# Performance work log

Measured on AMD Instinct MI355X. Metric: run time of the kernel, lower is better.

The kernel has to match this reference:

```python
import jax, jax.numpy as jnp
import numpy as np
from functools import partial

IM_H, IM_W = 1024, 1024
PRE_NMS = 1000
POST_NMS = 1000
FPN_POST_NMS = 1000
NMS_THRESH = 0.7
MIN_SIZE = 0.0
XFORM_CLIP = float(np.log(1000.0 / 16.0))  # BoxCoder bbox_xform_clip
K_MIN, K_MAX, K0, S0 = 2, 5, 4, 224.0      # ROI->FPN level mapper
NEG_INF = -1.0e30
N_IMG = 8


def _make_anchors(H, W, stride, n_img):
    """Grid anchors in H,W,A order (matches permute(0,2,3,1) flattening)."""
    ratios = np.array([0.5, 1.0, 2.0])
    size = stride * 8.0
    ws = size * np.sqrt(1.0 / ratios)
    hs = size * np.sqrt(ratios)
    sx = (np.arange(W) + 0.5) * stride
    sy = (np.arange(H) + 0.5) * stride
    cx, cy = np.meshgrid(sx, sy)  # [H,W]
    x1 = cx[..., None] - ws / 2.0
    y1 = cy[..., None] - hs / 2.0
    x2 = cx[..., None] + ws / 2.0
    y2 = cy[..., None] + hs / 2.0
    anc = np.stack([x1, y1, x2, y2], -1).reshape(-1, 4).astype(np.float32)
    return jnp.asarray(np.broadcast_to(anc, (n_img,) + anc.shape).copy())


def setup_inputs() -> dict:
    key = jax.random.key(0)
    ks = jax.random.split(key, 6)
    inp = {
        "obj_p2": jax.random.normal(ks[0], (N_IMG, 3, 256, 256), jnp.float32),
        "obj_p3": jax.random.normal(ks[1], (N_IMG, 3, 128, 128), jnp.float32),
        "obj_p4": jax.random.normal(ks[2], (N_IMG, 3, 64, 64), jnp.float32),
        "breg_p2": jax.random.normal(ks[3], (N_IMG, 12, 256, 256), jnp.float32) * 0.25,
        "breg_p3": jax.random.normal(ks[4], (N_IMG, 12, 128, 128), jnp.float32) * 0.25,
        "breg_p4": jax.random.normal(ks[5], (N_IMG, 12, 64, 64), jnp.float32) * 0.25,
        "anchors_p2": _make_anchors(256, 256, 4, N_IMG),
        "anchors_p3": _make_anchors(128, 128, 8, N_IMG),
        "anchors_p4": _make_anchors(64, 64, 16, N_IMG),
    }
    return inp


def _decode(deltas, anchors):
    # BoxCoder(weights=(1,1,1,1)) decode with the detectron +1 convention
    w = anchors[..., 2] - anchors[..., 0] + 1.0
    h = anchors[..., 3] - anchors[..., 1] + 1.0
    cx = anchors[..., 0] + 0.5 * w
    cy = anchors[..., 1] + 0.5 * h
    dx, dy = deltas[..., 0], deltas[..., 1]
    dw = jnp.minimum(deltas[..., 2], XFORM_CLIP)
    dh = jnp.minimum(deltas[..., 3], XFORM_CLIP)
    pcx = dx * w + cx
    pcy = dy * h + cy
    pw = jnp.exp(dw) * w
    ph = jnp.exp(dh) * h
    return jnp.stack(
        [pcx - 0.5 * pw, pcy - 0.5 * ph, pcx + 0.5 * pw - 1.0, pcy + 0.5 * ph - 1.0], -1
    )


def _nms_keep(boxes, valid, thresh):
    # boxes [K,4] already sorted by score desc; greedy hard NMS -> keep mask
    x1, y1, x2, y2 = boxes[:, 0], boxes[:, 1], boxes[:, 2], boxes[:, 3]
    areas = (x2 - x1 + 1.0) * (y2 - y1 + 1.0)
    xx1 = jnp.maximum(x1[:, None], x1[None, :])
    yy1 = jnp.maximum(y1[:, None], y1[None, :])
    xx2 = jnp.minimum(x2[:, None], x2[None, :])
    yy2 = jnp.minimum(y2[:, None], y2[None, :])
    inter = jnp.clip(xx2 - xx1 + 1.0, 0.0) * jnp.clip(yy2 - yy1 + 1.0, 0.0)
    iou = inter / (areas[:, None] + areas[None, :] - inter)
    K = boxes.shape[0]
    js = jnp.arange(K)

    def body(i, keep):
        sup = keep[i] & (iou[i] > thresh) & (js > i)
        return keep & ~sup

    return jax.lax.fori_loop(0, K, body, valid)


def _per_level(obj, breg, anchors):
    N, A, H, W = obj.shape
    scores = jax.nn.sigmoid(obj.transpose(0, 2, 3, 1).reshape(N, -1))  # [N, HWA]
    deltas = breg.reshape(N, A, 4, H, W).transpose(0, 3, 4, 1, 2).reshape(N, -1, 4)
    k = min(PRE_NMS, scores.shape[1])
    s, idx = jax.lax.top_k(scores, k)  # sorted desc
    d = jnp.take_along_axis(deltas, idx[..., None], axis=1)
    a = jnp.take_along_axis(anchors, idx[..., None], axis=1)
    p = _decode(d, a)
    # clip to image (width-1 / height-1)
    p = jnp.stack(
        [
            jnp.clip(p[..., 0], 0.0, IM_W - 1.0),
            jnp.clip(p[..., 1], 0.0, IM_H - 1.0),
            jnp.clip(p[..., 2], 0.0, IM_W - 1.0),
            jnp.clip(p[..., 3], 0.0, IM_H - 1.0),
        ],
        -1,
    )
    ws = p[..., 2] - p[..., 0] + 1.0
    hs = p[..., 3] - p[..., 1] + 1.0
    xc = p[..., 0] + ws / 2.0
    yc = p[..., 1] + hs / 2.0
    valid = (ws >= MIN_SIZE) & (hs >= MIN_SIZE) & (xc < IM_W) & (yc < IM_H)
    keep = jax.vmap(partial(_nms_keep, thresh=NMS_THRESH))(p, valid)
    ms = jnp.where(keep, s, NEG_INF)
    s2, i2 = jax.lax.top_k(ms, min(POST_NMS, k))
    b2 = jnp.take_along_axis(p, i2[..., None], axis=1)
    return b2, s2


def reference(obj_p2, obj_p3, obj_p4, breg_p2, breg_p3, breg_p4,
              anchors_p2, anchors_p3, anchors_p4):
    levels_in = [
        (obj_p2, breg_p2, anchors_p2),
        (obj_p3, breg_p3, anchors_p3),
        (obj_p4, breg_p4, anchors_p4),
    ]
    bs, ss = zip(*[_per_level(o, b, a) for o, b, a in levels_in])
    boxes = jnp.concatenate(bs, axis=1)   # [N, L*POST_NMS, 4]
    scores = jnp.concatenate(ss, axis=1)  # [N, L*POST_NMS]
    pk = min(FPN_POST_NMS, scores.shape[1])
    fs, fi = jax.lax.top_k(scores, pk)    # per-image inference-mode topk
    fb = jnp.take_along_axis(boxes, fi[..., None], axis=1)
    # ROI -> FPN level mapping
    area = (fb[..., 2] - fb[..., 0] + 1.0) * (fb[..., 3] - fb[..., 1] + 1.0)
    lvl = jnp.floor(K0 + jnp.log2(jnp.sqrt(area) / S0 + 1e-6))
    lvl = jnp.clip(lvl, K_MIN, K_MAX).astype(jnp.int32)
    return fb, fs, lvl
```

## Files before the change

kernel.cpp:

```cpp
#include <hip/hip_runtime.h>

#define NTASK 24
#define KSEL 1000
#define NIMG 8
#define NEG_INF_D (-1e30)
#define SEG 192
#define SORTN 2048


static __device__ __forceinline__ unsigned fkey(float x) {
    unsigned u = __float_as_uint(x);
    return u ^ ((u >> 31) ? 0xFFFFFFFFu : 0x80000000u);
}

static __device__ __forceinline__ float fkey_inv(unsigned key) {
    unsigned u = (key >> 31) ? (key ^ 0x80000000u) : ~key;
    return __uint_as_float(u);
}

static __device__ __forceinline__ unsigned long long dkey(double d) {
    unsigned long long u = (unsigned long long)__double_as_longlong(d);
    if (u >> 63) u = ~u; else u |= 0x8000000000000000ull;
    return u;
}

static __device__ __forceinline__ int level_hw(int lvl) {
    return lvl == 0 ? 65536 : (lvl == 1 ? 16384 : 4096);
}


__global__ __launch_bounds__(256) void k_zero(uint4* __restrict__ p, int n16) {
    const int t = blockIdx.x * 256 + threadIdx.x;
    if (t < n16) p[t] = make_uint4(0u, 0u, 0u, 0u);
}


__global__ __launch_bounds__(256) void k_hist(const float* __restrict__ o2,
                                              const float* __restrict__ o3,
                                              const float* __restrict__ o4,
                                              unsigned* __restrict__ hist) {
    const int task = blockIdx.x, img = task / 3, lvl = task % 3;
    const float* obj = lvl == 0 ? o2 : (lvl == 1 ? o3 : o4);
    const int HW = level_hw(lvl);
    const int total = 3 * HW;
    const float* base = obj + (size_t)img * total;
    const int tid = threadIdx.x;

    __shared__ unsigned h[4096];
    for (int t = tid; t < 4096; t += 256) h[t] = 0u;
    __syncthreads();

    const int per4 = (total / 32) >> 2;
    const int beg4 = blockIdx.y * per4;
    const float4* base4 = (const float4*)base;
    for (int t = beg4 + tid; t < beg4 + per4; t += 256) {
        float4 v = base4[t];
        atomicAdd(&h[fkey(v.x) >> 20], 1u);
        atomicAdd(&h[fkey(v.y) >> 20], 1u);
        atomicAdd(&h[fkey(v.z) >> 20], 1u);
        atomicAdd(&h[fkey(v.w) >> 20], 1u);
    }
    __syncthreads();

    unsigned* H = hist + task * 4096;
    for (int t = tid; t < 4096; t += 256)
        if (h[t]) atomicAdd(&H[t], h[t]);
}


__global__ __launch_bounds__(256) void k_thresh(const unsigned* __restrict__ hist,
                                                int* __restrict__ thrBin) {
    const int task = blockIdx.x, tid = threadIdx.x;
    __shared__ unsigned h[4096];
    __shared__ unsigned part[256];
    const unsigned* H = hist + task * 4096;
    for (int t = tid; t < 4096; t += 256) h[t] = H[t];
    __syncthreads();
    unsigned s = 0;
    for (int q = 0; q < 16; ++q) s += h[tid * 16 + q];
    part[tid] = s;
    __syncthreads();
    if (tid == 0) {
        unsigned cum = 0;
        int c = 255;
        for (; c >= 0; --c) {
            if (cum + part[c] >= (unsigned)KSEL) break;
            cum += part[c];
        }
        if (c < 0) c = 0;
        int bin = 0;
        for (int b = c * 16 + 15; b >= c * 16; --b) {
            if (cum + h[b] >= (unsigned)KSEL) { bin = b; break; }
            cum += h[b];
        }
        thrBin[task] = bin;
    }
}


__global__ __launch_bounds__(256) void k_compact(const float* __restrict__ o2,
                                                 const float* __restrict__ o3,
                                                 const float* __restrict__ o4,
                                                 const int* __restrict__ thrBin,
                                                 int* __restrict__ cntB,
                                                 unsigned long long* __restrict__ cand) {
    const int task = blockIdx.x, img = task / 3, lvl = task % 3;
    const float* obj = lvl == 0 ? o2 : (lvl == 1 ? o3 : o4);
    const int HW = level_hw(lvl);
    const int total = 3 * HW;
    const float* base = obj + (size_t)img * total;
    const unsigned B = (unsigned)thrBin[task];

    __shared__ unsigned long long buf[256];
    __shared__ unsigned scnt;
    if (threadIdx.x == 0) scnt = 0u;
    __syncthreads();

    const int per4 = (total / 32) >> 2;
    const int beg4 = blockIdx.y * per4;
    const float4* base4 = (const float4*)base;
    for (int t = beg4 + threadIdx.x; t < beg4 + per4; t += 256) {
        float4 v = base4[t];
        const int e0 = t * 4;
#pragma unroll
        for (int q = 0; q < 4; ++q) {
            float x = q == 0 ? v.x : (q == 1 ? v.y : (q == 2 ? v.z : v.w));
            unsigned key = fkey(x);
            if ((key >> 20) >= B) {
                unsigned s = atomicAdd(&scnt, 1u);
                if (s < 256u) {
                    int el = e0 + q;
                    int a = el / HW, pos = el - a * HW;
                    int i = pos * 3 + a;
                    buf[s] = ((unsigned long long)key << 32) | (unsigned)(~(unsigned)i);
                }
            }
        }
    }
    __syncthreads();
    int n = (int)scnt; if (n > SEG) n = SEG;
    const int seg = task * 32 + blockIdx.y;
    if (threadIdx.x == 0) cntB[seg] = n;
    unsigned long long* C = cand + (size_t)seg * SEG;
    for (int t = threadIdx.x; t < n; t += 256) C[t] = buf[t];
}


__global__ __launch_bounds__(1024) void k_sel(const int* __restrict__ cntB,
                                              const unsigned long long* __restrict__ cand,
                                              unsigned long long* __restrict__ sorted64) {
    const int task = blockIdx.x, tid = threadIdx.x;
    const int wid = tid >> 6, lane = tid & 63;
    __shared__ unsigned long long comp[SORTN];
    __shared__ int pref[33];

    if (tid == 0) {
        int p = 0;
        for (int s = 0; s < 32; ++s) { pref[s] = p; p += cntB[task * 32 + s]; }
        pref[32] = p;
    }
    for (int t = tid; t < SORTN; t += 1024) comp[t] = 0ull;
    __syncthreads();

    for (int s = wid; s < 32; s += 16) {
        const int b = pref[s], n = pref[s + 1] - b;
        const unsigned long long* C = cand + (size_t)(task * 32 + s) * SEG;
        for (int k = lane; k < n; k += 64)
            if (b + k < SORTN) comp[b + k] = C[k];
    }
    __syncthreads();

    for (unsigned k = 2; k <= SORTN; k <<= 1) {
        for (unsigned j = k >> 1; j > 0; j >>= 1) {
            for (unsigned i = tid; i < SORTN; i += 1024) {
                unsigned ixj = i ^ j;
                if (ixj > i) {
                    unsigned long long A = comp[i], Bv = comp[ixj];
                    bool desc = ((i & k) == 0);
                    if ((A < Bv) == desc) { comp[i] = Bv; comp[ixj] = A; }
                }
            }
            __syncthreads();
        }
    }

    for (int t = tid; t < KSEL; t += 1024) sorted64[task * KSEL + t] = comp[t];
}


__global__ __launch_bounds__(128) void k_decode(
    const unsigned long long* __restrict__ sorted64,
    const float* __restrict__ g2, const float* __restrict__ g3, const float* __restrict__ g4,
    const float* __restrict__ a2, const float* __restrict__ a3, const float* __restrict__ a4,
    double* __restrict__ boxes, double* __restrict__ score, int* __restrict__ valid) {

    const int task = blockIdx.x, img = task / 3, lvl = task % 3;
    const int r = blockIdx.y * 125 + threadIdx.x;
    if (threadIdx.x >= 125) return;

    const float* brg = lvl == 0 ? g2 : (lvl == 1 ? g3 : g4);
    const float* anc = lvl == 0 ? a2 : (lvl == 1 ? a3 : a4);
    const int HW = level_hw(lvl);
    const int N = HW * 3;
    const double XC = 4.135166556742356;

    unsigned long long e = sorted64[task * KSEL + r];
    unsigned key = (unsigned)(e >> 32);
    int i = (int)(~(unsigned)(e & 0xFFFFFFFFull));
    int a = i % 3, pos = i / 3;

    double x = (double)fkey_inv(key);
    double s = 1.0 / (1.0 + exp(-x));

    const float* bb = brg + (size_t)img * 12 * HW + (size_t)(a * 4) * HW + pos;
    double dx = (double)bb[0];
    double dy = (double)bb[(size_t)HW];
    double dw = (double)bb[(size_t)2 * HW];
    double dh = (double)bb[(size_t)3 * HW];

    const float* an = anc + ((size_t)img * N + (size_t)i) * 4;
    double ax1 = an[0], ay1 = an[1], ax2 = an[2], ay2 = an[3];

    double w = ax2 - ax1 + 1.0, h = ay2 - ay1 + 1.0;
    double cx = ax1 + 0.5 * w, cy = ay1 + 0.5 * h;
    if (dw > XC) dw = XC;
    if (dh > XC) dh = XC;
    double pcx = dx * w + cx, pcy = dy * h + cy;
    double pw = exp(dw) * w, ph = exp(dh) * h;
    double x1 = pcx - 0.5 * pw, y1 = pcy - 0.5 * ph;
    double x2 = pcx + 0.5 * pw - 1.0, y2 = pcy + 0.5 * ph - 1.0;
    x1 = fmin(fmax(x1, 0.0), 1023.0);
    y1 = fmin(fmax(y1, 0.0), 1023.0);
    x2 = fmin(fmax(x2, 0.0), 1023.0);
    y2 = fmin(fmax(y2, 0.0), 1023.0);
    double ws_ = x2 - x1 + 1.0, hs_ = y2 - y1 + 1.0;
    double xc = x1 + ws_ / 2.0, yc = y1 + hs_ / 2.0;
    int v = (ws_ >= 0.0) && (hs_ >= 0.0) && (xc < 1024.0) && (yc < 1024.0);

    double* bo = boxes + (size_t)(task * KSEL + r) * 4;
    bo[0] = x1; bo[1] = y1; bo[2] = x2; bo[3] = y2;
    score[task * KSEL + r] = s;
    valid[task * KSEL + r] = v;
}


__global__ __launch_bounds__(512) void k_mask(const double* __restrict__ boxes,
                                              unsigned long long* __restrict__ maskT) {
    const int task = blockIdx.x;
    const int wid = threadIdx.x >> 6, lane = threadIdx.x & 63;
    const int t = blockIdx.y * 8 + wid;
    if (t >= 136) return;
    int I = 0, rem = t;
    while (rem >= 16 - I) { rem -= 16 - I; ++I; }
    const int J = I + rem;

    const double* B = boxes + (size_t)task * KSEL * 4;
    const int j = J * 64 + lane;
    const int jc = j < KSEL ? j : KSEL - 1;
    double jx1 = B[jc * 4 + 0], jy1 = B[jc * 4 + 1];
    double jx2 = B[jc * 4 + 2], jy2 = B[jc * 4 + 3];
    double aj = (jx2 - jx1 + 1.0) * (jy2 - jy1 + 1.0);

    unsigned long long* MT = maskT + (size_t)task * 16000 + (size_t)J * KSEL;
    int iend = I * 64 + 64; if (iend > KSEL) iend = KSEL;
    for (int i = I * 64; i < iend; ++i) {
        double ix1 = B[i * 4 + 0], iy1 = B[i * 4 + 1];
        double ix2 = B[i * 4 + 2], iy2 = B[i * 4 + 3];
        double ai = (ix2 - ix1 + 1.0) * (iy2 - iy1 + 1.0);
        double xx1 = fmax(ix1, jx1), yy1 = fmax(iy1, jy1);
        double xx2 = fmin(ix2, jx2), yy2 = fmin(iy2, jy2);
        double iw = xx2 - xx1 + 1.0; iw = iw > 0.0 ? iw : 0.0;
        double ih = yy2 - yy1 + 1.0; ih = ih > 0.0 ? ih : 0.0;
        double inter = iw * ih;
        double iou = inter / (ai + aj - inter);
        bool sup = (j > i) && (j < KSEL) && (iou > 0.7);
        unsigned long long m = __ballot(sup);
        if (lane == 0) MT[i] = m;
    }
}


__global__ __launch_bounds__(1024) void k_nms(const unsigned long long* __restrict__ maskT,
                                              const int* __restrict__ valid,
                                              const double* __restrict__ score,
                                              int* __restrict__ order, double* __restrict__ s2) {
    const int task = blockIdx.x;
    const int tid = threadIdx.x;
    const int wid = tid >> 6, lane = tid & 63;

    __shared__ unsigned long long Msh[16000];
    __shared__ unsigned long long kws[16];
    __shared__ int prefK[16], prefN[16], totKsh;

    {
        const ulonglong2* MG = (const ulonglong2*)(maskT + (size_t)task * 16000);
        ulonglong2* ML = (ulonglong2*)Msh;
        for (int t = tid; t < 8000; t += 1024) ML[t] = MG[t];
    }
    if (tid < 16) kws[tid] = 0ull;
    __syncthreads();
    if (tid < KSEL && valid[task * KSEL + tid])
        atomicOr(&kws[tid >> 6], 1ull << (tid & 63));
    __syncthreads();

    for (int p = 0; p < 16; ++p) {
        if (p > 0 && wid >= p) {
            unsigned long long kp = kws[p - 1];
            unsigned long long m = ((kp >> lane) & 1ull) ? Msh[wid * KSEL + (p - 1) * 64 + lane] : 0ull;
            if (m) atomicAnd(&kws[wid], ~m);
        }
        if (wid == p) {
            __threadfence_block();
            const int row = p * 64 + lane;
            unsigned long long m = (row < KSEL) ? Msh[p * KSEL + row] : 0ull;
            unsigned long long k = kws[p];
            unsigned long long processed = 0ull;
            while (true) {
                unsigned long long sup = __ballot((m & k) != 0ull);
                unsigned long long rem = k & sup & ~processed;
                if (!rem) break;
                int b = __ffsll((long long)rem) - 1;
                unsigned lo = (unsigned)__builtin_amdgcn_readlane((int)(unsigned)(m & 0xFFFFFFFFull), b);
                unsigned hi = (unsigned)__builtin_amdgcn_readlane((int)(unsigned)(m >> 32), b);
                unsigned long long vict = ((unsigned long long)hi << 32) | lo;
                k &= ~vict;
                processed = (1ull << b) | ((1ull << b) - 1ull);
            }
            if (lane == 0) kws[p] = k;
        }
        __syncthreads();
    }

    if (tid == 0) {
        int pk = 0, pn = 0;
        for (int l = 0; l < 16; ++l) {
            prefK[l] = pk; prefN[l] = pn;
            int limit = KSEL - 64 * l; if (limit > 64) limit = 64;
            int kb = (int)__popcll(kws[l]);
            pk += kb; pn += limit - kb;
        }
        totKsh = pk;
    }
    __syncthreads();

    if (tid < 16) {
        unsigned long long kw = kws[tid];
        int limit = KSEL - 64 * tid; if (limit > 64) limit = 64;
        int ck = prefK[tid], cn = totKsh + prefN[tid];
        for (int b = 0; b < limit; ++b) {
            int j = tid * 64 + b;
            if ((kw >> b) & 1ull) {
                order[task * KSEL + ck] = j;
                s2[task * KSEL + ck] = score[task * KSEL + j];
                ++ck;
            } else {
                order[task * KSEL + cn] = j;
                s2[task * KSEL + cn] = NEG_INF_D;
                ++cn;
            }
        }
    }
}


__global__ __launch_bounds__(1024) void k_final(const double* __restrict__ boxes,
                                                const double* __restrict__ s2,
                                                const int* __restrict__ order,
                                                float* __restrict__ out) {
    const int img = blockIdx.x;
    const int tid = threadIdx.x;
    __shared__ unsigned long long Mkey[KSEL];
    __shared__ int Mid[KSEL];

    const double* L0 = s2 + (size_t)(img * 3 + 0) * KSEL;
    const double* L1 = s2 + (size_t)(img * 3 + 1) * KSEL;
    const double* L2 = s2 + (size_t)(img * 3 + 2) * KSEL;

    if (tid < KSEL) {
        const int r = tid;
        int lo = 0, hi = r;
        while (lo < hi) {
            int a = (lo + hi) >> 1;
            if (dkey(L0[a]) >= dkey(L1[r - 1 - a])) lo = a + 1; else hi = a;
        }
        int a = lo, b = r - a;
        unsigned long long ka = dkey(L0[a]), kb = dkey(L1[b]);
        if (ka >= kb) { Mkey[r] = ka; Mid[r] = a; }
        else          { Mkey[r] = kb; Mid[r] = 1000 + b; }
    }
    __syncthreads();

    if (tid < KSEL) {
        const int r = tid;
        int lo = 0, hi = r;
        while (lo < hi) {
            int a = (lo + hi) >> 1;
            if (Mkey[a] >= dkey(L2[r - 1 - a])) lo = a + 1; else hi = a;
        }
        int a = lo, b = r - a;
        int e;
        if (a < KSEL && Mkey[a] >= dkey(L2[b])) e = Mid[a];
        else e = 2000 + b;

        int l = e / 1000, rr = e - l * 1000;
        int task = img * 3 + l;
        int pos = order[task * KSEL + rr];
        const double* bo = boxes + (size_t)(task * KSEL + pos) * 4;
        double b0 = bo[0], b1 = bo[1], b2 = bo[2], b3 = bo[3];
        double s = s2[task * KSEL + rr];

        float* fb = out + ((size_t)img * KSEL + r) * 4;
        fb[0] = (float)b0; fb[1] = (float)b1; fb[2] = (float)b2; fb[3] = (float)b3;
        out[8 * KSEL * 4 + img * KSEL + r] = (float)s;

        double area = (b2 - b0 + 1.0) * (b3 - b1 + 1.0);
        double lv = floor(4.0 + log2(sqrt(area) / 224.0 + 1e-6));
        if (!(lv >= 2.0)) lv = 2.0;
        if (lv > 5.0) lv = 5.0;
        out[8 * KSEL * 5 + img * KSEL + r] = (float)lv;
    }
}


extern "C" void kernel_launch(void* const* d_in, const int* in_sizes, int n_in,
                              void* d_out, int out_size, void* d_ws, size_t ws_size,
                              hipStream_t stream) {
    const float* o2 = (const float*)d_in[0];
    const float* o3 = (const float*)d_in[1];
    const float* o4 = (const float*)d_in[2];
    const float* g2 = (const float*)d_in[3];
    const float* g3 = (const float*)d_in[4];
    const float* g4 = (const float*)d_in[5];
    const float* a2 = (const float*)d_in[6];
    const float* a3 = (const float*)d_in[7];
    const float* a4 = (const float*)d_in[8];

    char* ws = (char*)d_ws;
    int*                valid = (int*)(ws + 96000);
    double*             score = (double*)(ws + 192000);
    double*             boxes = (double*)(ws + 384000);
    int*                order = (int*)(ws + 1152000);
    double*             s2    = (double*)(ws + 1248000);
    char*               scr   = ws + 1440000;

    unsigned*           hist     = (unsigned*)(scr + 0);
    int*                thrBin   = (int*)(scr + 393216);
    int*                cntB     = (int*)(scr + 393312);
    unsigned long long* cand     = (unsigned long long*)(scr + 396384);
    unsigned long long* sorted64 = (unsigned long long*)(scr + 1600000);
    unsigned long long* maskT    = (unsigned long long*)scr;

    k_zero<<<96, 256, 0, stream>>>((uint4*)scr, 24576);

    k_hist<<<dim3(NTASK, 32), 256, 0, stream>>>(o2, o3, o4, hist);
    k_thresh<<<NTASK, 256, 0, stream>>>(hist, thrBin);
    k_compact<<<dim3(NTASK, 32), 256, 0, stream>>>(o2, o3, o4, thrBin, cntB, cand);
    k_sel<<<NTASK, 1024, 0, stream>>>(cntB, cand, sorted64);
    k_decode<<<dim3(NTASK, 8), 128, 0, stream>>>(sorted64, g2, g3, g4, a2, a3, a4,
                                                 boxes, score, valid);
    k_mask<<<dim3(NTASK, 17), 512, 0, stream>>>(boxes, maskT);
    k_nms<<<NTASK, 1024, 0, stream>>>(maskT, valid, score, order, s2);
    k_final<<<NIMG, 1024, 0, stream>>>(boxes, s2, order, (float*)d_out);
}
```

Baseline: 116.3 us.

## Fuse threshold into compact and box decode into IoU mask kernel

The threshold-bin search moves into k_compact, so each of the 32 blocks per task redoes the histogram scan instead of waiting on a separate launch. Box decode moves into the IoU mask kernel: each wavefront decodes its row and column tiles itself and broadcasts row boxes with warp shuffles instead of reading them back from global memory. This drops two kernel launches and a global round trip for the boxes. The cost is redundant decode work, up to 16 times per box, plus repeated 16KB histogram loads per block. The sorted buffer also moves to a new workspace offset.

```diff
diff --git a/kernel.cpp b/kernel.cpp
--- a/kernel.cpp
+++ b/kernel.cpp
@@ -26,6 +26,54 @@
 
 static __device__ __forceinline__ int level_hw(int lvl) {
     return lvl == 0 ? 65536 : (lvl == 1 ? 16384 : 4096);
+}
+
+static __device__ __forceinline__ double shfl_d(double v, int src) {
+    return __shfl(v, src, 64);
+}
+
+static __device__ __forceinline__ void decode_box(
+    int img, int lvl, int task, int r,
+    const unsigned long long* __restrict__ sorted64,
+    const float* __restrict__ brg, const float* __restrict__ anc,
+    double& x1, double& y1, double& x2, double& y2, double& s, int& v) {
+
+    const int HW = level_hw(lvl);
+    const int N = HW * 3;
+    const double XC = 4.135166556742356;
+
+    unsigned long long e = sorted64[task * KSEL + r];
+    unsigned key = (unsigned)(e >> 32);
+    int i = (int)(~(unsigned)(e & 0xFFFFFFFFull));
+    int a = i % 3, pos = i / 3;
+
+    double x = (double)fkey_inv(key);
+    s = 1.0 / (1.0 + exp(-x));
+
+    const float* bb = brg + (size_t)img * 12 * HW + (size_t)(a * 4) * HW + pos;
+    double dx = (double)bb[0];
+    double dy = (double)bb[(size_t)HW];
+    double dw = (double)bb[(size_t)2 * HW];
+    double dh = (double)bb[(size_t)3 * HW];
+
+    const float* an = anc + ((size_t)img * N + (size_t)i) * 4;
+    double ax1 = an[0], ay1 = an[1], ax2 = an[2], ay2 = an[3];
+
+    double w = ax2 - ax1 + 1.0, h = ay2 - ay1 + 1.0;
+    double cx = ax1 + 0.5 * w, cy = ay1 + 0.5 * h;
+    if (dw > XC) dw = XC;
+    if (dh > XC) dh = XC;
+    double pcx = dx * w + cx, pcy = dy * h + cy;
+    double pw = exp(dw) * w, ph = exp(dh) * h;
+    x1 = pcx - 0.5 * pw; y1 = pcy - 0.5 * ph;
+    x2 = pcx + 0.5 * pw - 1.0; y2 = pcy + 0.5 * ph - 1.0;
+    x1 = fmin(fmax(x1, 0.0), 1023.0);
+    y1 = fmin(fmax(y1, 0.0), 1023.0);
+    x2 = fmin(fmax(x2, 0.0), 1023.0);
+    y2 = fmin(fmax(y2, 0.0), 1023.0);
+    double ws_ = x2 - x1 + 1.0, hs_ = y2 - y1 + 1.0;
+    double xc = x1 + ws_ / 2.0, yc = y1 + hs_ / 2.0;
+    v = (ws_ >= 0.0) && (hs_ >= 0.0) && (xc < 1024.0) && (yc < 1024.0);
 }
 
 
@@ -68,40 +116,10 @@
 }
 
 
-__global__ __launch_bounds__(256) void k_thresh(const unsigned* __restrict__ hist,
-                                                int* __restrict__ thrBin) {
-    const int task = blockIdx.x, tid = threadIdx.x;
-    __shared__ unsigned h[4096];
-    __shared__ unsigned part[256];
-    const unsigned* H = hist + task * 4096;
-    for (int t = tid; t < 4096; t += 256) h[t] = H[t];
-    __syncthreads();
-    unsigned s = 0;
-    for (int q = 0; q < 16; ++q) s += h[tid * 16 + q];
-    part[tid] = s;
-    __syncthreads();
-    if (tid == 0) {
-        unsigned cum = 0;
-        int c = 255;
-        for (; c >= 0; --c) {
-            if (cum + part[c] >= (unsigned)KSEL) break;
-            cum += part[c];
-        }
-        if (c < 0) c = 0;
-        int bin = 0;
-        for (int b = c * 16 + 15; b >= c * 16; --b) {
-            if (cum + h[b] >= (unsigned)KSEL) { bin = b; break; }
-            cum += h[b];
-        }
-        thrBin[task] = bin;
-    }
-}
-
-
 __global__ __launch_bounds__(256) void k_compact(const float* __restrict__ o2,
                                                  const float* __restrict__ o3,
                                                  const float* __restrict__ o4,
-                                                 const int* __restrict__ thrBin,
+                                                 const unsigned* __restrict__ hist,
                                                  int* __restrict__ cntB,
                                                  unsigned long long* __restrict__ cand) {
     const int task = blockIdx.x, img = task / 3, lvl = task % 3;
@@ -109,17 +127,44 @@
     const int HW = level_hw(lvl);
     const int total = 3 * HW;
     const float* base = obj + (size_t)img * total;
-    const unsigned B = (unsigned)thrBin[task];
-
+    const int tid = threadIdx.x;
+
+    __shared__ unsigned h[4096];
+    __shared__ unsigned part[256];
+    __shared__ int sBin;
     __shared__ unsigned long long buf[256];
     __shared__ unsigned scnt;
-    if (threadIdx.x == 0) scnt = 0u;
-    __syncthreads();
+
+    const unsigned* H = hist + task * 4096;
+    for (int t = tid; t < 4096; t += 256) h[t] = H[t];
+    if (tid == 0) scnt = 0u;
+    __syncthreads();
+    unsigned sacc = 0;
+    for (int q = 0; q < 16; ++q) sacc += h[tid * 16 + q];
+    part[tid] = sacc;
+    __syncthreads();
+    if (tid == 0) {
+        unsigned cum = 0;
+        int c = 255;
+        for (; c >= 0; --c) {
+            if (cum + part[c] >= (unsigned)KSEL) break;
+            cum += part[c];
+        }
+        if (c < 0) c = 0;
+        int bin = 0;
+        for (int b = c * 16 + 15; b >= c * 16; --b) {
+            if (cum + h[b] >= (unsigned)KSEL) { bin = b; break; }
+            cum += h[b];
+        }
+        sBin = bin;
+    }
+    __syncthreads();
+    const unsigned B = (unsigned)sBin;
 
     const int per4 = (total / 32) >> 2;
     const int beg4 = blockIdx.y * per4;
     const float4* base4 = (const float4*)base;
-    for (int t = beg4 + threadIdx.x; t < beg4 + per4; t += 256) {
+    for (int t = beg4 + tid; t < beg4 + per4; t += 256) {
         float4 v = base4[t];
         const int e0 = t * 4;
 #pragma unroll
@@ -140,9 +185,9 @@
     __syncthreads();
     int n = (int)scnt; if (n > SEG) n = SEG;
     const int seg = task * 32 + blockIdx.y;
-    if (threadIdx.x == 0) cntB[seg] = n;
+    if (tid == 0) cntB[seg] = n;
     unsigned long long* C = cand + (size_t)seg * SEG;
-    for (int t = threadIdx.x; t < n; t += 256) C[t] = buf[t];
+    for (int t = tid; t < n; t += 256) C[t] = buf[t];
 }
 
 
@@ -188,65 +233,14 @@
 }
 
 
-__global__ __launch_bounds__(128) void k_decode(
+__global__ __launch_bounds__(512) void k_maskdec(
     const unsigned long long* __restrict__ sorted64,
     const float* __restrict__ g2, const float* __restrict__ g3, const float* __restrict__ g4,
     const float* __restrict__ a2, const float* __restrict__ a3, const float* __restrict__ a4,
-    double* __restrict__ boxes, double* __restrict__ score, int* __restrict__ valid) {
+    double* __restrict__ boxes, double* __restrict__ score, int* __restrict__ valid,
+    unsigned long long* __restrict__ maskT) {
 
     const int task = blockIdx.x, img = task / 3, lvl = task % 3;
-    const int r = blockIdx.y * 125 + threadIdx.x;
-    if (threadIdx.x >= 125) return;
-
-    const float* brg = lvl == 0 ? g2 : (lvl == 1 ? g3 : g4);
-    const float* anc = lvl == 0 ? a2 : (lvl == 1 ? a3 : a4);
-    const int HW = level_hw(lvl);
-    const int N = HW * 3;
-    const double XC = 4.135166556742356;
-
-    unsigned long long e = sorted64[task * KSEL + r];
-    unsigned key = (unsigned)(e >> 32);
-    int i = (int)(~(unsigned)(e & 0xFFFFFFFFull));
-    int a = i % 3, pos = i / 3;
-
-    double x = (double)fkey_inv(key);
-    double s = 1.0 / (1.0 + exp(-x));
-
-    const float* bb = brg + (size_t)img * 12 * HW + (size_t)(a * 4) * HW + pos;
-    double dx = (double)bb[0];
-    double dy = (double)bb[(size_t)HW];
-    double dw = (double)bb[(size_t)2 * HW];
-    double dh = (double)bb[(size_t)3 * HW];
-
-    const float* an = anc + ((size_t)img * N + (size_t)i) * 4;
-    double ax1 = an[0], ay1 = an[1], ax2 = an[2], ay2 = an[3];
-
-    double w = ax2 - ax1 + 1.0, h = ay2 - ay1 + 1.0;
-    double cx = ax1 + 0.5 * w, cy = ay1 + 0.5 * h;
-    if (dw > XC) dw = XC;
-    if (dh > XC) dh = XC;
-    double pcx = dx * w + cx, pcy = dy * h + cy;
-    double pw = exp(dw) * w, ph = exp(dh) * h;
-    double x1 = pcx - 0.5 * pw, y1 = pcy - 0.5 * ph;
-    double x2 = pcx + 0.5 * pw - 1.0, y2 = pcy + 0.5 * ph - 1.0;
-    x1 = fmin(fmax(x1, 0.0), 1023.0);
-    y1 = fmin(fmax(y1, 0.0), 1023.0);
-    x2 = fmin(fmax(x2, 0.0), 1023.0);
-    y2 = fmin(fmax(y2, 0.0), 1023.0);
-    double ws_ = x2 - x1 + 1.0, hs_ = y2 - y1 + 1.0;
-    double xc = x1 + ws_ / 2.0, yc = y1 + hs_ / 2.0;
-    int v = (ws_ >= 0.0) && (hs_ >= 0.0) && (xc < 1024.0) && (yc < 1024.0);
-
-    double* bo = boxes + (size_t)(task * KSEL + r) * 4;
-    bo[0] = x1; bo[1] = y1; bo[2] = x2; bo[3] = y2;
-    score[task * KSEL + r] = s;
-    valid[task * KSEL + r] = v;
-}
-
-
-__global__ __launch_bounds__(512) void k_mask(const double* __restrict__ boxes,
-                                              unsigned long long* __restrict__ maskT) {
-    const int task = blockIdx.x;
     const int wid = threadIdx.x >> 6, lane = threadIdx.x & 63;
     const int t = blockIdx.y * 8 + wid;
     if (t >= 136) return;
@@ -254,18 +248,36 @@
     while (rem >= 16 - I) { rem -= 16 - I; ++I; }
     const int J = I + rem;
 
-    const double* B = boxes + (size_t)task * KSEL * 4;
+    const float* brg = lvl == 0 ? g2 : (lvl == 1 ? g3 : g4);
+    const float* anc = lvl == 0 ? a2 : (lvl == 1 ? a3 : a4);
+
     const int j = J * 64 + lane;
     const int jc = j < KSEL ? j : KSEL - 1;
-    double jx1 = B[jc * 4 + 0], jy1 = B[jc * 4 + 1];
-    double jx2 = B[jc * 4 + 2], jy2 = B[jc * 4 + 3];
+    double jx1, jy1, jx2, jy2, js; int jv;
+    decode_box(img, lvl, task, jc, sorted64, brg, anc, jx1, jy1, jx2, jy2, js, jv);
     double aj = (jx2 - jx1 + 1.0) * (jy2 - jy1 + 1.0);
+
+    const int ri = I * 64 + lane;
+    double tix1, tiy1, tix2, tiy2, tis; int tiv;
+    if (I == J) { tix1 = jx1; tiy1 = jy1; tix2 = jx2; tiy2 = jy2; tis = js; tiv = jv; }
+    else {
+        const int ric = ri < KSEL ? ri : KSEL - 1;
+        decode_box(img, lvl, task, ric, sorted64, brg, anc, tix1, tiy1, tix2, tiy2, tis, tiv);
+    }
+
+    if (I == J && ri < KSEL) {
+        double* bo = boxes + (size_t)(task * KSEL + ri) * 4;
+        bo[0] = jx1; bo[1] = jy1; bo[2] = jx2; bo[3] = jy2;
+        score[task * KSEL + ri] = js;
+        valid[task * KSEL + ri] = jv;
+    }
 
     unsigned long long* MT = maskT + (size_t)task * 16000 + (size_t)J * KSEL;
     int iend = I * 64 + 64; if (iend > KSEL) iend = KSEL;
     for (int i = I * 64; i < iend; ++i) {
-        double ix1 = B[i * 4 + 0], iy1 = B[i * 4 + 1];
-        double ix2 = B[i * 4 + 2], iy2 = B[i * 4 + 3];
+        const int src = i & 63;
+        double ix1 = shfl_d(tix1, src), iy1 = shfl_d(tiy1, src);
+        double ix2 = shfl_d(tix2, src), iy2 = shfl_d(tiy2, src);
         double ai = (ix2 - ix1 + 1.0) * (iy2 - iy1 + 1.0);
         double xx1 = fmax(ix1, jx1), yy1 = fmax(iy1, jy1);
         double xx2 = fmin(ix2, jx2), yy2 = fmin(iy2, jy2);
@@ -348,13 +360,13 @@
         int limit = KSEL - 64 * tid; if (limit > 64) limit = 64;
         int ck = prefK[tid], cn = totKsh + prefN[tid];
         for (int b = 0; b < limit; ++b) {
-            int j = tid * 64 + b;
+            int jj = tid * 64 + b;
             if ((kw >> b) & 1ull) {
-                order[task * KSEL + ck] = j;
-                s2[task * KSEL + ck] = score[task * KSEL + j];
+                order[task * KSEL + ck] = jj;
+                s2[task * KSEL + ck] = score[task * KSEL + jj];
                 ++ck;
             } else {
-                order[task * KSEL + cn] = j;
+                order[task * KSEL + cn] = jj;
                 s2[task * KSEL + cn] = NEG_INF_D;
                 ++cn;
             }
@@ -443,22 +455,20 @@
     double*             s2    = (double*)(ws + 1248000);
     char*               scr   = ws + 1440000;
 
-    unsigned*           hist     = (unsigned*)(scr + 0);
-    int*                thrBin   = (int*)(scr + 393216);
-    int*                cntB     = (int*)(scr + 393312);
-    unsigned long long* cand     = (unsigned long long*)(scr + 396384);
-    unsigned long long* sorted64 = (unsigned long long*)(scr + 1600000);
-    unsigned long long* maskT    = (unsigned long long*)scr;
+    unsigned long long* sorted64 = (unsigned long long*)(ws + 1152000);
+
+    unsigned*           hist  = (unsigned*)(scr + 0);
+    int*                cntB  = (int*)(scr + 393216);
+    unsigned long long* cand  = (unsigned long long*)(scr + 396288);
+    unsigned long long* maskT = (unsigned long long*)scr;
 
     k_zero<<<96, 256, 0, stream>>>((uint4*)scr, 24576);
 
     k_hist<<<dim3(NTASK, 32), 256, 0, stream>>>(o2, o3, o4, hist);
-    k_thresh<<<NTASK, 256, 0, stream>>>(hist, thrBin);
-    k_compact<<<dim3(NTASK, 32), 256, 0, stream>>>(o2, o3, o4, thrBin, cntB, cand);
+    k_compact<<<dim3(NTASK, 32), 256, 0, stream>>>(o2, o3, o4, hist, cntB, cand);
     k_sel<<<NTASK, 1024, 0, stream>>>(cntB, cand, sorted64);
-    k_decode<<<dim3(NTASK, 8), 128, 0, stream>>>(sorted64, g2, g3, g4, a2, a3, a4,
-                                                 boxes, score, valid);
-    k_mask<<<dim3(NTASK, 17), 512, 0, stream>>>(boxes, maskT);
+    k_maskdec<<<dim3(NTASK, 17), 512, 0, stream>>>(sorted64, g2, g3, g4, a2, a3, a4,
+                                                   boxes, score, valid, maskT);
     k_nms<<<NTASK, 1024, 0, stream>>>(maskT, valid, score, order, s2);
     k_final<<<NIMG, 1024, 0, stream>>>(boxes, s2, order, (float*)d_out);
 }
```

After: 117.1 us. About the same (+0.7%).
